# Performance work log

Measured on AMD Instinct MI355X. Metric: run time of the kernel, lower is better.

Reference implementation:

```python
import jax, jax.numpy as jnp
import numpy as np

NEG_SLOPE = 0.2

def _leaky(x):
    return jnp.where(x >= 0, x, NEG_SLOPE * x)

def _unigat(X, W, b, ae, av, pair_e, pair_v, num_v, num_e):
    # theta
    Xp = X @ W + b                                                    # [N, d]
    # v2e mean aggregation -> hyperedge features
    deg_e = jax.ops.segment_sum(jnp.ones(pair_e.shape, jnp.float32), pair_e, num_segments=num_e)
    Y = jax.ops.segment_sum(Xp[pair_v], pair_e, num_segments=num_e) / jnp.maximum(deg_e, 1.0)[:, None]  # [E, d]
    # GAT-style attention per incidence pair (edge term + node term), dropout=identity in eval
    s = _leaky((Y @ ae)[pair_e] + (Xp @ av)[pair_v])                  # [P]
    # segment softmax over edges incident to each node
    m = jax.ops.segment_max(s, pair_v, num_segments=num_v)
    ex = jnp.exp(s - m[pair_v])
    den = jax.ops.segment_sum(ex, pair_v, num_segments=num_v)
    alpha = ex / den[pair_v]                                          # [P]
    out = jax.ops.segment_sum(alpha[:, None] * Y[pair_e], pair_v, num_segments=num_v)  # [N, d]
    return jax.nn.elu(out)  # is_last=False everywhere -> ELU (use_bn=False)

def _multi_head(X, W, b, ae, av, pair_e, pair_v, num_v, num_e):
    # W:[H,din,d] b:[H,d] ae/av:[H,d]; concat heads on feature dim
    f = lambda Wh, bh, aeh, avh: _unigat(X, Wh, bh, aeh, avh, pair_e, pair_v, num_v, num_e)
    outs = jax.vmap(f)(W, b, ae, av)                                  # [H, N, d]
    return jnp.transpose(outs, (1, 0, 2)).reshape(X.shape[0], -1)     # [N, H*d]

def setup_inputs() -> dict:
    key = jax.random.key(0)
    ks = jax.random.split(key, 12)
    N, E, P = 100000, 20000, 1600000
    din, dh, H, C = 128, 64, 4, 40
    concat = 2
    inp = {
        "x0": jax.random.normal(ks[0], (N, din), jnp.float32),
        "x1": jax.random.normal(ks[1], (N, din), jnp.float32),
        "W1": jax.random.normal(ks[2], (H, din, dh), jnp.float32) * 0.05,
        "b1": jnp.zeros((H, dh), jnp.float32),
        "ae1": jax.random.normal(ks[3], (H, dh), jnp.float32) * 0.05,
        "av1": jax.random.normal(ks[4], (H, dh), jnp.float32) * 0.05,
        "W2": jax.random.normal(ks[5], (concat * dh * H, C), jnp.float32) * 0.05,
        "b2": jnp.zeros((C,), jnp.float32),
        "ae2": jax.random.normal(ks[6], (C,), jnp.float32) * 0.05,
        "av2": jax.random.normal(ks[7], (C,), jnp.float32) * 0.05,
        "pair_e": jax.random.randint(ks[8], (P,), 0, E, jnp.int32),
        "pair_v": jax.random.randint(ks[9], (P,), 0, N, jnp.int32),
        "num_v": N,
        "num_e": E,
    }
    return inp

def reference(x0, x1, W1, b1, ae1, av1, W2, b2, ae2, av2, pair_e, pair_v, num_v, num_e):
    # dropout layers are identity in eval mode
    h0 = _multi_head(x0, W1, b1, ae1, av1, pair_e, pair_v, num_v, num_e)
    h1 = _multi_head(x1, W1, b1, ae1, av1, pair_e, pair_v, num_v, num_e)
    h = jnp.concatenate([h0, h1], axis=-1)                            # [N, concat*H*dh]
    return _unigat(h, W2, b2, ae2, av2, pair_e, pair_v, num_v, num_e) # [N, C]
```

## Files before the change

### kernel.cpp

```cpp
#include <hip/hip_runtime.h>
#include <cstdint>
#include <cstddef>

static constexpr int DIN = 128;
static constexpr int DH = 64;
static constexpr int NH = 4;
static constexpr int DCAT = 512;
static constexpr int NC = 40;
static constexpr int E_CONST = 20000;
static constexpr int SH_V = 9, SUBD_V = 512;
static constexpr int SH_E = 7, SUBD_E = 128;
static constexpr int CHUNKA = 4096;

typedef unsigned short u16;
typedef __attribute__((ext_vector_type(4))) unsigned short u16x4;
typedef __attribute__((ext_vector_type(8))) unsigned short u16x8;
typedef __attribute__((ext_vector_type(8))) short bf16x8;
typedef __attribute__((ext_vector_type(4))) float f32x4;

static __device__ __forceinline__ float bf2f(u16 u) {
    union { unsigned int i; float f; } x;
    x.i = ((unsigned int)u) << 16;
    return x.f;
}
static __device__ __forceinline__ u16 f2bf(float f) {
    union { float f; unsigned int i; } x;
    x.f = f;
    unsigned int r = x.i + 0x7fffu + ((x.i >> 16) & 1u);
    return (u16)(r >> 16);
}


__global__ void k_hist2(const int* __restrict__ pv, const int* __restrict__ pe,
                        int* __restrict__ btot_v, int* __restrict__ btot_e, int P) {
    __shared__ int cv[256], ce[256];
    int tid = threadIdx.x;
    cv[tid] = 0; ce[tid] = 0;
    __syncthreads();
    int p0 = blockIdx.x * CHUNKA;
    #pragma unroll
    for (int j = 0; j < CHUNKA / 256; ++j) {
        int p = p0 + tid + j * 256;
        if (p < P) {
            atomicAdd(&cv[pv[p] >> SH_V], 1);
            atomicAdd(&ce[pe[p] >> SH_E], 1);
        }
    }
    __syncthreads();
    if (cv[tid]) atomicAdd(&btot_v[tid], cv[tid]);
    if (ce[tid]) atomicAdd(&btot_e[tid], ce[tid]);
}

__global__ void k_scan_small(int* __restrict__ a, int n) {
    __shared__ int wsum[16];
    __shared__ int carry_s;
    int tid = threadIdx.x;
    int lane = tid & 63;
    int w = tid >> 6;
    if (tid == 0) carry_s = 0;
    __syncthreads();
    for (int base = 0; base < n; base += 1024) {
        int i = base + tid;
        int v = (i < n) ? a[i] : 0;
        int x = v;
        #pragma unroll
        for (int off = 1; off < 64; off <<= 1) {
            int t = __shfl_up(x, off);
            if (lane >= off) x += t;
        }
        if (lane == 63) wsum[w] = x;
        __syncthreads();
        int woff = 0;
        for (int k = 0; k < w; ++k) woff += wsum[k];
        int carry = carry_s;
        if (i < n) a[i] = carry + woff + x - v;
        int tot = 0;
        for (int k = 0; k < 16; ++k) tot += wsum[k];
        __syncthreads();
        if (tid == 0) carry_s = carry + tot;
        __syncthreads();
    }
    if (tid == 0) a[n] = carry_s;
}

__global__ void k_scatter2way(const int* __restrict__ pv, const int* __restrict__ pe,
                              const int* __restrict__ bstart_v, const int* __restrict__ bstart_e,
                              int* __restrict__ cur_v, int* __restrict__ cur_e,
                              uint2* __restrict__ sorted_v, uint2* __restrict__ sorted_e, int P) {
    __shared__ int cv[256], ce[256], posv[256], pose[256];
    int tid = threadIdx.x;
    cv[tid] = 0; ce[tid] = 0;
    __syncthreads();
    int p0 = blockIdx.x * CHUNKA;
    int kv[CHUNKA / 256], ke[CHUNKA / 256];
    #pragma unroll
    for (int j = 0; j < CHUNKA / 256; ++j) {
        int p = p0 + tid + j * 256;
        if (p < P) {
            kv[j] = pv[p];
            ke[j] = pe[p];
            atomicAdd(&cv[kv[j] >> SH_V], 1);
            atomicAdd(&ce[ke[j] >> SH_E], 1);
        } else {
            kv[j] = -1;
            ke[j] = -1;
        }
    }
    __syncthreads();
    if (cv[tid]) posv[tid] = bstart_v[tid] + atomicAdd(&cur_v[tid], cv[tid]);
    if (ce[tid]) pose[tid] = bstart_e[tid] + atomicAdd(&cur_e[tid], ce[tid]);
    __syncthreads();
    #pragma unroll
    for (int j = 0; j < CHUNKA / 256; ++j) {
        if (kv[j] >= 0) {
            int iv = atomicAdd(&posv[kv[j] >> SH_V], 1);
            sorted_v[iv] = make_uint2((unsigned)kv[j], (unsigned)ke[j]);
            int ie = atomicAdd(&pose[ke[j] >> SH_E], 1);
            sorted_e[ie] = make_uint2((unsigned)ke[j], (unsigned)kv[j]);
        }
    }
}

template <int SUBD, int SH>
__global__ void k_build(const uint2* __restrict__ sorted, const int* __restrict__ bstart,
                        int* __restrict__ start_out, int* __restrict__ deg_out,
                        int* __restrict__ csr_out, int D) {
    __shared__ int deg[SUBD], pos[SUBD];
    int b = blockIdx.x;
    int tid = threadIdx.x;
    int base_key = b << SH;
    int s0 = bstart[b];
    int cnt = bstart[b + 1] - s0;
    for (int k = tid; k < SUBD; k += 256) deg[k] = 0;
    __syncthreads();
    for (int i = tid; i < cnt; i += 256)
        atomicAdd(&deg[(int)sorted[s0 + i].x - base_key], 1);
    __syncthreads();
    if (tid < 64) {
        int carry = 0;
        for (int base = 0; base < SUBD; base += 64) {
            int d = deg[base + tid];
            int x = d;
            #pragma unroll
            for (int off = 1; off < 64; off <<= 1) {
                int t = __shfl_up(x, off);
                if (tid >= off) x += t;
            }
            pos[base + tid] = carry + x - d;
            carry += __shfl(x, 63);
        }
    }
    __syncthreads();
    for (int k = tid; k < SUBD; k += 256) {
        int key = base_key + k;
        if (key < D) {
            start_out[key] = s0 + pos[k];
            deg_out[key] = deg[k];
        }
    }
    __syncthreads();
    for (int i = tid; i < cnt; i += 256) {
        uint2 pr = sorted[s0 + i];
        int loc = (int)pr.x - base_key;
        int idx = atomicAdd(&pos[loc], 1);
        csr_out[s0 + idx] = (int)pr.y;
    }
}


__global__ void k_wav(const float* __restrict__ W1, const float* __restrict__ b1,
                      const float* __restrict__ av1, float* __restrict__ wav,
                      float* __restrict__ bav) {
    int h = blockIdx.x;
    int k = threadIdx.x;
    float s = 0.f;
    for (int j = 0; j < DH; ++j) s += W1[(size_t)(h * DIN + k) * DH + j] * av1[h * DH + j];
    wav[h * DIN + k] = s;
    if (k == 0) {
        float t = 0.f;
        for (int j = 0; j < DH; ++j) t += b1[h * DH + j] * av1[h * DH + j];
        bav[h] = t;
    }
}

__global__ void k_build_wcatT(const float* __restrict__ W1, u16* __restrict__ WcatT) {
    int idx = blockIdx.x * 256 + threadIdx.x;
    if (idx >= 256 * DIN) return;
    int c = idx >> 7, k = idx & 127;
    int h = c >> 6, j = c & 63;
    WcatT[c * DIN + k] = f2bf(W1[((size_t)h * DIN + k) * DH + j]);
}

__global__ void k_build_w2T(const float* __restrict__ W2, u16* __restrict__ W2T) {
    int idx = blockIdx.x * 256 + threadIdx.x;
    if (idx >= 48 * DCAT) return;
    int c = idx >> 9, k = idx & 511;
    float v = (c < NC) ? W2[(size_t)k * NC + c] : 0.f;
    W2T[c * DCAT + k] = f2bf(v);
}

__global__ void k_conv(const float* __restrict__ X0, const float* __restrict__ X1,
                       const float* __restrict__ wav, const float* __restrict__ bav,
                       u16* __restrict__ Xbi, float* __restrict__ sv8, int N) {
    int wave = (blockIdx.x * blockDim.x + threadIdx.x) >> 6;
    int lane = threadIdx.x & 63;
    if (wave >= N) return;
    int xz = blockIdx.y;
    const float* X = xz ? X1 : X0;
    float2 a = *(const float2*)(X + (size_t)wave * DIN + lane * 2);
    unsigned int packed = (unsigned int)f2bf(a.x) | ((unsigned int)f2bf(a.y) << 16);
    *(unsigned int*)(Xbi + (size_t)wave * 256 + xz * 128 + lane * 2) = packed;
    float s[NH];
    #pragma unroll
    for (int h = 0; h < NH; ++h) {
        float2 wv = *(const float2*)(wav + h * DIN + lane * 2);
        float t = a.x * wv.x + a.y * wv.y;
        #pragma unroll
        for (int off = 32; off >= 1; off >>= 1) t += __shfl_xor(t, off);
        s[h] = t;
    }
    if (lane == 0) {
        #pragma unroll
        for (int h = 0; h < NH; ++h) sv8[(size_t)wave * 8 + h * 2 + xz] = s[h] + bav[h];
    }
}

__global__ void k_edge_mean1(const u16* __restrict__ Xbi, const int* __restrict__ start_e,
                             const int* __restrict__ deg_e, const int* __restrict__ csr_e_v,
                             u16* __restrict__ Xbar0, u16* __restrict__ Xbar1, int E) {
    int wave = (blockIdx.x * blockDim.x + threadIdx.x) >> 6;
    int lane = threadIdx.x & 63;
    if (wave >= E) return;
    int s = start_e[wave], t = s + deg_e[wave];
    int q = lane >> 4, c = lane & 15;
    float a0[8], a1[8];
    #pragma unroll
    for (int j = 0; j < 8; ++j) { a0[j] = 0.f; a1[j] = 0.f; }
    int i = s + q;
    u16x8 y0A = {0}, y1A = {0}, y0B = {0}, y1B = {0}, y0C = {0}, y1C = {0};
#define EM1_LOAD(Y0, Y1, IDX) { int v_ = csr_e_v[IDX]; \
        const u16* yp_ = Xbi + (size_t)v_ * 256 + c * 8; \
        Y0 = *(const u16x8*)yp_; Y1 = *(const u16x8*)(yp_ + 128); }
#define EM1_CONSUME(Y0, Y1) { \
        _Pragma("unroll") \
        for (int j = 0; j < 8; ++j) { a0[j] += bf2f(Y0[j]); a1[j] += bf2f(Y1[j]); } }
    if (i < t) EM1_LOAD(y0A, y1A, i);
    if (i + 4 < t) EM1_LOAD(y0B, y1B, i + 4);
    if (i + 8 < t) EM1_LOAD(y0C, y1C, i + 8);
    for (; i + 8 < t; i += 12) {
        EM1_CONSUME(y0A, y1A);
        if (i + 12 < t) EM1_LOAD(y0A, y1A, i + 12);
        EM1_CONSUME(y0B, y1B);
        if (i + 16 < t) EM1_LOAD(y0B, y1B, i + 16);
        EM1_CONSUME(y0C, y1C);
        if (i + 20 < t) EM1_LOAD(y0C, y1C, i + 20);
    }
    if (i < t) EM1_CONSUME(y0A, y1A);
    if (i + 4 < t) EM1_CONSUME(y0B, y1B);
#undef EM1_LOAD
#undef EM1_CONSUME
    #pragma unroll
    for (int j = 0; j < 8; ++j) {
        a0[j] += __shfl_xor(a0[j], 16);
        a0[j] += __shfl_xor(a0[j], 32);
        a1[j] += __shfl_xor(a1[j], 16);
        a1[j] += __shfl_xor(a1[j], 32);
    }
    int deg = t - s;
    float inv = 1.f / (float)(deg > 1 ? deg : 1);
    if (q == 0) {
        u16x8 r0, r1;
        #pragma unroll
        for (int j = 0; j < 8; ++j) { r0[j] = f2bf(a0[j] * inv); r1[j] = f2bf(a1[j] * inv); }
        *(u16x8*)(Xbar0 + (size_t)wave * DIN + c * 8) = r0;
        *(u16x8*)(Xbar1 + (size_t)wave * DIN + c * 8) = r1;
    }
}

template <int KDIM, int NTILES, int DOTMODE>
__global__ __launch_bounds__(256) void k_gemm_mfma(const u16* __restrict__ A0,
                                                   const u16* __restrict__ A1, int M,
                                                   const u16* __restrict__ Bt,
                                                   const float* __restrict__ bias,
                                                   u16* __restrict__ out0, u16* __restrict__ out1,
                                                   int ldo, int ncols,
                                                   const float* __restrict__ dvec,
                                                   float* __restrict__ dout) {
    constexpr int LDB = KDIM + 8;
    __shared__ u16 Bs[NTILES * 16 * LDB];
    const u16* A = blockIdx.z ? A1 : A0;
    u16* out = blockIdx.z ? out1 : out0;
    int tid = threadIdx.x;
    int colbase = blockIdx.y * NTILES * 16;
    const u16* Btblk = Bt + (size_t)colbase * KDIM;
    for (int idx = tid * 4; idx < NTILES * 16 * KDIM; idx += 256 * 4) {
        int c = idx / KDIM, k = idx % KDIM;
        *(u16x4*)&Bs[c * LDB + k] = *(const u16x4*)(Btblk + c * KDIM + k);
    }
    __syncthreads();
    int w = tid >> 6, lane = tid & 63;
    int r0 = blockIdx.x * 64 + w * 16;
    int arow = r0 + (lane & 15);
    bool avalid = arow < M;
    const u16* ap = A + (size_t)arow * KDIM + (lane >> 4) * 8;
    f32x4 acc[NTILES];
    #pragma unroll
    for (int nt = 0; nt < NTILES; ++nt) acc[nt] = (f32x4){0.f, 0.f, 0.f, 0.f};
    #pragma unroll
    for (int k0 = 0; k0 < KDIM; k0 += 32) {
        bf16x8 a = (bf16x8)(short)0;
        if (avalid) a = *(const bf16x8*)(ap + k0);
        #pragma unroll
        for (int nt = 0; nt < NTILES; ++nt) {
            bf16x8 b = *(const bf16x8*)&Bs[(nt * 16 + (lane & 15)) * LDB + k0 + (lane >> 4) * 8];
            acc[nt] = __builtin_amdgcn_mfma_f32_16x16x32_bf16(a, b, acc[nt], 0, 0, 0);
        }
    }
    #pragma unroll
    for (int j = 0; j < 4; ++j) {
        int row = r0 + (lane >> 4) * 4 + j;
        float pA = 0.f, pB = 0.f;
        #pragma unroll
        for (int nt = 0; nt < NTILES; ++nt) {
            int col = colbase + nt * 16 + (lane & 15);
            bool cok = col < ncols;
            float val = cok ? acc[nt][j] + bias[col] : 0.f;
            if (DOTMODE == 1) {
                float dv = dvec[col];
                if (nt < NTILES / 2) pA += val * dv; else pB += val * dv;
            } else if (DOTMODE == 2) {
                pA += cok ? val * dvec[col] : 0.f;
            }
            if (row < M && cok) out[(size_t)row * ldo + col] = f2bf(val);
        }
        if (DOTMODE) {
            pA += __shfl_xor(pA, 1);
            pA += __shfl_xor(pA, 2);
            pA += __shfl_xor(pA, 4);
            pA += __shfl_xor(pA, 8);
            if (DOTMODE == 1) {
                pB += __shfl_xor(pB, 1);
                pB += __shfl_xor(pB, 2);
                pB += __shfl_xor(pB, 4);
                pB += __shfl_xor(pB, 8);
            }
            if ((lane & 15) == 0 && row < M) {
                if (DOTMODE == 1) {
                    int hbase = blockIdx.y * 2;
                    int z = blockIdx.z;
                    dout[(size_t)row * 8 + hbase * 2 + z] = pA;
                    dout[(size_t)row * 8 + (hbase + 1) * 2 + z] = pB;
                } else {
                    dout[row] = pA;
                }
            }
        }
    }
}

__global__ void k_node_pass1(const u16* __restrict__ Ycat, const float* __restrict__ se8,
                             const float* __restrict__ sv8, const int* __restrict__ start_v,
                             const int* __restrict__ deg_v, const int* __restrict__ csr_v_e,
                             u16* __restrict__ hbuf, int N) {
    int wave = (blockIdx.x * blockDim.x + threadIdx.x) >> 6;
    int lane = threadIdx.x & 63;
    if (wave >= N) return;
    int p0 = start_v[wave], p1 = p0 + deg_v[wave];
    int g = lane >> 5;
    int c = lane & 31;
    int h = c >> 3;
    u16* orow = hbuf + (size_t)wave * DCAT + c * 8;
    if (p1 == p0) {
        if (g == 0) {
            u16x8 z8 = {0, 0, 0, 0, 0, 0, 0, 0};
            *(u16x8*)orow = z8;
            *(u16x8*)(orow + 256) = z8;
        }
        return;
    }
    float sv0 = sv8[(size_t)wave * 8 + h * 2];
    float sv1 = sv8[(size_t)wave * 8 + h * 2 + 1];
    float den0 = 0.f, den1 = 0.f;
    float a0[8], a1[8];
    #pragma unroll
    for (int j = 0; j < 8; ++j) { a0[j] = 0.f; a1[j] = 0.f; }
    for (int i = p0 + g; i < p1; i += 2) {
        int e = csr_v_e[i];
        float2 s2 = *(const float2*)(se8 + e * 8 + h * 2);
        float x0 = s2.x + sv0;
        float x1 = s2.y + sv1;
        x0 = fmaxf(x0, 0.2f * x0);
        x1 = fmaxf(x1, 0.2f * x1);
        float e0 = __expf(x0);
        float e1 = __expf(x1);
        den0 += e0;
        den1 += e1;
        const u16* yp = Ycat + (size_t)e * 512 + c * 8;
        u16x8 q0 = *(const u16x8*)yp;
        u16x8 q1 = *(const u16x8*)(yp + 256);
        #pragma unroll
        for (int j = 0; j < 8; ++j) { a0[j] += e0 * bf2f(q0[j]); a1[j] += e1 * bf2f(q1[j]); }
    }
    den0 += __shfl_xor(den0, 32);
    den1 += __shfl_xor(den1, 32);
    #pragma unroll
    for (int j = 0; j < 8; ++j) {
        a0[j] += __shfl_xor(a0[j], 32);
        a1[j] += __shfl_xor(a1[j], 32);
    }
    float i0 = 1.f / den0, i1 = 1.f / den1;
    u16x8 r0, r1;
    #pragma unroll
    for (int j = 0; j < 8; ++j) {
        float o0 = a0[j] * i0;
        float o1 = a1[j] * i1;
        o0 = o0 > 0.f ? o0 : __expf(o0) - 1.f;
        o1 = o1 > 0.f ? o1 : __expf(o1) - 1.f;
        r0[j] = f2bf(o0);
        r1[j] = f2bf(o1);
    }
    if (g == 0) {
        *(u16x8*)orow = r0;
        *(u16x8*)(orow + 256) = r1;
    }
}


__global__ void k_edge_mean2(const u16* __restrict__ Xp2b, const int* __restrict__ start_e,
                             const int* __restrict__ deg_ea, const int* __restrict__ csr_e_v,
                             u16* __restrict__ Y2b, const float* __restrict__ ae2,
                             float* __restrict__ se2, int E) {
    int wave = (blockIdx.x * blockDim.x + threadIdx.x) >> 6;
    int lane = threadIdx.x & 63;
    if (wave >= E) return;
    int s = start_e[wave], t = s + deg_ea[wave];
    int g = lane >> 4, c = lane & 15;
    bool act = c < 10;
    float acc[4];
    #pragma unroll
    for (int j = 0; j < 4; ++j) acc[j] = 0.f;
    for (int i = s + g; i < t; i += 4) {
        int v = csr_e_v[i];
        if (act) {
            u16x4 y = *(const u16x4*)(Xp2b + (size_t)v * NC + c * 4);
            acc[0] += bf2f(y.x);
            acc[1] += bf2f(y.y);
            acc[2] += bf2f(y.z);
            acc[3] += bf2f(y.w);
        }
    }
    #pragma unroll
    for (int j = 0; j < 4; ++j) {
        acc[j] += __shfl_xor(acc[j], 16);
        acc[j] += __shfl_xor(acc[j], 32);
    }
    int deg = t - s;
    float inv = 1.f / (float)(deg > 1 ? deg : 1);
    float p = 0.f;
    if (act) {
        float4 ae = *(const float4*)(ae2 + c * 4);
        float y0 = acc[0] * inv, y1 = acc[1] * inv, y2 = acc[2] * inv, y3 = acc[3] * inv;
        p = y0 * ae.x + y1 * ae.y + y2 * ae.z + y3 * ae.w;
        if (g == 0) {
            u16x4 r = {f2bf(y0), f2bf(y1), f2bf(y2), f2bf(y3)};
            *(u16x4*)(Y2b + (size_t)wave * NC + c * 4) = r;
        }
    }
    #pragma unroll
    for (int off = 8; off >= 1; off >>= 1) p += __shfl_xor(p, off);
    if (lane == 0) se2[wave] = p;
}

__global__ void k_node_pass2(const u16* __restrict__ Y2b, const float* __restrict__ se2,
                             const float* __restrict__ sv2, const int* __restrict__ start_v,
                             const int* __restrict__ deg_va, const int* __restrict__ csr_v_e,
                             float* __restrict__ out, int N) {
    int wave = (blockIdx.x * blockDim.x + threadIdx.x) >> 6;
    int lane = threadIdx.x & 63;
    if (wave >= N) return;
    int s = start_v[wave], t = s + deg_va[wave];
    int g = lane >> 4, c = lane & 15;
    bool act = c < 10;
    float* orow = out + (size_t)wave * NC;
    if (t == s) {
        if (g == 0 && act) *(float4*)(orow + c * 4) = make_float4(0.f, 0.f, 0.f, 0.f);
        return;
    }
    float svv = sv2[wave];
    float den = 0.f;
    float acc[4];
    #pragma unroll
    for (int j = 0; j < 4; ++j) acc[j] = 0.f;
    for (int i = s + g; i < t; i += 4) {
        int e = csr_v_e[i];
        float x = se2[e] + svv;
        x = fmaxf(x, 0.2f * x);
        float ex = __expf(x);
        den += ex;
        if (act) {
            u16x4 y = *(const u16x4*)(Y2b + (size_t)e * NC + c * 4);
            acc[0] += ex * bf2f(y.x);
            acc[1] += ex * bf2f(y.y);
            acc[2] += ex * bf2f(y.z);
            acc[3] += ex * bf2f(y.w);
        }
    }
    den += __shfl_xor(den, 16);
    den += __shfl_xor(den, 32);
    #pragma unroll
    for (int j = 0; j < 4; ++j) {
        acc[j] += __shfl_xor(acc[j], 16);
        acc[j] += __shfl_xor(acc[j], 32);
    }
    if (g == 0 && act) {
        float inv = 1.f / den;
        float4 o;
        float* op = &o.x;
        #pragma unroll
        for (int j = 0; j < 4; ++j) {
            float v = acc[j] * inv;
            op[j] = v > 0.f ? v : __expf(v) - 1.f;
        }
        *(float4*)(orow + c * 4) = o;
    }
}

extern "C" void kernel_launch(void* const* d_in, const int* in_sizes, int n_in,
                              void* d_out, int out_size, void* d_ws, size_t ws_size,
                              hipStream_t stream) {
    const float* x0 = (const float*)d_in[0];
    const float* x1 = (const float*)d_in[1];
    const float* W1 = (const float*)d_in[2];
    const float* b1 = (const float*)d_in[3];
    const float* ae1 = (const float*)d_in[4];
    const float* av1 = (const float*)d_in[5];
    const float* W2 = (const float*)d_in[6];
    const float* b2 = (const float*)d_in[7];
    const float* ae2 = (const float*)d_in[8];
    const float* av2 = (const float*)d_in[9];
    const int* pe = (const int*)d_in[10];
    const int* pv = (const int*)d_in[11];

    const int N = in_sizes[0] / DIN;
    const int P = in_sizes[10];
    const int E = E_CONST;
    const int NBKT_V = (N + SUBD_V - 1) / SUBD_V;
    const int NBKT_E = (E + SUBD_E - 1) / SUBD_E;

    char* base = (char*)d_ws;
    auto alloc = [&](size_t bytes) -> void* {
        void* p = (void*)base;
        base += (bytes + 255) & ~(size_t)255;
        return p;
    };
    u16* Xbi = (u16*)alloc((size_t)N * 256 * 2);
    u16* hbuf = (u16*)alloc((size_t)N * DCAT * 2);
    u16* Xbar0 = (u16*)alloc((size_t)E * DIN * 2);
    u16* Xbar1 = (u16*)alloc((size_t)E * DIN * 2);
    u16* Ycat = (u16*)alloc((size_t)E * 512 * 2);
    u16* Xp2b = (u16*)alloc((size_t)N * NC * 2);
    u16* Y2b = (u16*)alloc((size_t)E * NC * 2);
    float* se8 = (float*)alloc((size_t)E * 8 * 4);
    float* se2 = (float*)alloc((size_t)E * 4);
    float* sv8 = (float*)alloc((size_t)N * 8 * 4);
    float* sv2 = (float*)alloc((size_t)N * 4);
    float* wav = (float*)alloc((size_t)NH * DIN * 4);
    float* bav = (float*)alloc((size_t)NH * 4);
    u16* WcatT = (u16*)alloc((size_t)256 * DIN * 2);
    u16* W2T = (u16*)alloc((size_t)48 * DCAT * 2);
    uint2* sorted_v = (uint2*)alloc((size_t)P * 8);
    uint2* sorted_e = (uint2*)alloc((size_t)P * 8);
    int* start_v = (int*)alloc((size_t)N * 4);
    int* deg_v = (int*)alloc((size_t)N * 4);
    int* start_e = (int*)alloc((size_t)E * 4);
    int* deg_e = (int*)alloc((size_t)E * 4);
    int* csr_v_e = (int*)alloc((size_t)P * 4);
    int* csr_e_v = (int*)alloc((size_t)P * 4);
    char* zstart = base;
    int* bstart_v = (int*)alloc((size_t)(NBKT_V + 1) * 4);
    int* bstart_e = (int*)alloc((size_t)(NBKT_E + 1) * 4);
    int* cur_v = (int*)alloc((size_t)256 * 4);
    int* cur_e = (int*)alloc((size_t)256 * 4);
    size_t zbytes = (size_t)(base - zstart);

    if ((size_t)(base - (char*)d_ws) > ws_size) return;

    hipMemsetAsync(zstart, 0, zbytes, stream);

    dim3 b256(256);
    int nA = (P + CHUNKA - 1) / CHUNKA;
    k_hist2<<<nA, b256, 0, stream>>>(pv, pe, bstart_v, bstart_e, P);
    k_scan_small<<<1, 1024, 0, stream>>>(bstart_v, NBKT_V);
    k_scan_small<<<1, 1024, 0, stream>>>(bstart_e, NBKT_E);
    k_scatter2way<<<nA, b256, 0, stream>>>(pv, pe, bstart_v, bstart_e, cur_v, cur_e,
                                           sorted_v, sorted_e, P);
    k_build<SUBD_V, SH_V><<<NBKT_V, b256, 0, stream>>>(sorted_v, bstart_v, start_v, deg_v,
                                                       csr_v_e, N);
    k_build<SUBD_E, SH_E><<<NBKT_E, b256, 0, stream>>>(sorted_e, bstart_e, start_e, deg_e,
                                                       csr_e_v, E);

    k_wav<<<NH, DIN, 0, stream>>>(W1, b1, av1, wav, bav);
    k_build_wcatT<<<(256 * DIN + 255) / 256, b256, 0, stream>>>(W1, WcatT);
    k_build_w2T<<<(48 * DCAT + 255) / 256, b256, 0, stream>>>(W2, W2T);

    int gN4 = (N + 3) / 4;
    int gE4 = (E + 3) / 4;
    dim3 gconv(gN4, 2);
    k_conv<<<gconv, b256, 0, stream>>>(x0, x1, wav, bav, Xbi, sv8, N);

    k_edge_mean1<<<gE4, b256, 0, stream>>>(Xbi, start_e, deg_e, csr_e_v, Xbar0, Xbar1, E);
    dim3 g1((E + 63) / 64, 2, 2);
    k_gemm_mfma<DIN, 8, 1><<<g1, b256, 0, stream>>>(Xbar0, Xbar1, E, WcatT, b1,
                                                    Ycat, Ycat + 256, 512, 256, ae1, se8);
    k_node_pass1<<<gN4, b256, 0, stream>>>(Ycat, se8, sv8, start_v, deg_v, csr_v_e, hbuf, N);

    dim3 g2((N + 63) / 64, 1, 1);
    k_gemm_mfma<DCAT, 3, 2><<<g2, b256, 0, stream>>>(hbuf, hbuf, N, W2T, b2, Xp2b, Xp2b,
                                                     NC, NC, av2, sv2);
    k_edge_mean2<<<gE4, b256, 0, stream>>>(Xp2b, start_e, deg_e, csr_e_v, Y2b, ae2, se2, E);
    k_node_pass2<<<gN4, b256, 0, stream>>>(Y2b, se2, sv2, start_v, deg_v, csr_v_e,
                                           (float*)d_out, N);
}
```

Baseline: 675.4 us.

## Sub-bucket CSR build by secondary key to order neighbor lists

```diff
diff --git a/kernel.cpp b/kernel.cpp
--- a/kernel.cpp
+++ b/kernel.cpp
@@ -10,6 +10,10 @@
 static constexpr int E_CONST = 20000;
 static constexpr int SH_V = 9, SUBD_V = 512;
 static constexpr int SH_E = 7, SUBD_E = 128;
+static constexpr int ECH = 11, NSUB_E = 10;
+static constexpr int VCH = 12, NSUB_V = 25;
+static constexpr int NKV = 196 * NSUB_E;
+static constexpr int NKE = 157 * NSUB_V;
 static constexpr int CHUNKA = 4096;
 
 typedef unsigned short u16;
@@ -29,26 +33,32 @@
     unsigned int r = x.i + 0x7fffu + ((x.i >> 16) & 1u);
     return (u16)(r >> 16);
 }
+static __device__ __forceinline__ int keyV(int v, int e) { return (v >> SH_V) * NSUB_E + (e >> ECH); }
+static __device__ __forceinline__ int keyE(int e, int v) { return (e >> SH_E) * NSUB_V + (v >> VCH); }
 
 
 __global__ void k_hist2(const int* __restrict__ pv, const int* __restrict__ pe,
                         int* __restrict__ btot_v, int* __restrict__ btot_e, int P) {
-    __shared__ int cv[256], ce[256];
+    __shared__ int cv[NKV], ce[NKE];
     int tid = threadIdx.x;
-    cv[tid] = 0; ce[tid] = 0;
+    for (int k = tid; k < NKV; k += 256) cv[k] = 0;
+    for (int k = tid; k < NKE; k += 256) ce[k] = 0;
     __syncthreads();
     int p0 = blockIdx.x * CHUNKA;
     #pragma unroll
     for (int j = 0; j < CHUNKA / 256; ++j) {
         int p = p0 + tid + j * 256;
         if (p < P) {
-            atomicAdd(&cv[pv[p] >> SH_V], 1);
-            atomicAdd(&ce[pe[p] >> SH_E], 1);
-        }
-    }
-    __syncthreads();
-    if (cv[tid]) atomicAdd(&btot_v[tid], cv[tid]);
-    if (ce[tid]) atomicAdd(&btot_e[tid], ce[tid]);
+            int v = pv[p], e = pe[p];
+            atomicAdd(&cv[keyV(v, e)], 1);
+            atomicAdd(&ce[keyE(e, v)], 1);
+        }
+    }
+    __syncthreads();
+    for (int k = tid; k < NKV; k += 256)
+        if (cv[k]) atomicAdd(&btot_v[k], cv[k]);
+    for (int k = tid; k < NKE; k += 256)
+        if (ce[k]) atomicAdd(&btot_e[k], ce[k]);
 }
 
 __global__ void k_scan_small(int* __restrict__ a, int n) {
@@ -87,9 +97,10 @@
                               const int* __restrict__ bstart_v, const int* __restrict__ bstart_e,
                               int* __restrict__ cur_v, int* __restrict__ cur_e,
                               uint2* __restrict__ sorted_v, uint2* __restrict__ sorted_e, int P) {
-    __shared__ int cv[256], ce[256], posv[256], pose[256];
+    __shared__ int cv[NKV], posv[NKV], ce[NKE], pose[NKE];
     int tid = threadIdx.x;
-    cv[tid] = 0; ce[tid] = 0;
+    for (int k = tid; k < NKV; k += 256) cv[k] = 0;
+    for (int k = tid; k < NKE; k += 256) ce[k] = 0;
     __syncthreads();
     int p0 = blockIdx.x * CHUNKA;
     int kv[CHUNKA / 256], ke[CHUNKA / 256];
@@ -99,29 +110,31 @@
         if (p < P) {
             kv[j] = pv[p];
             ke[j] = pe[p];
-            atomicAdd(&cv[kv[j] >> SH_V], 1);
-            atomicAdd(&ce[ke[j] >> SH_E], 1);
+            atomicAdd(&cv[keyV(kv[j], ke[j])], 1);
+            atomicAdd(&ce[keyE(ke[j], kv[j])], 1);
         } else {
             kv[j] = -1;
             ke[j] = -1;
         }
     }
     __syncthreads();
-    if (cv[tid]) posv[tid] = bstart_v[tid] + atomicAdd(&cur_v[tid], cv[tid]);
-    if (ce[tid]) pose[tid] = bstart_e[tid] + atomicAdd(&cur_e[tid], ce[tid]);
+    for (int k = tid; k < NKV; k += 256)
+        if (cv[k]) posv[k] = bstart_v[k] + atomicAdd(&cur_v[k], cv[k]);
+    for (int k = tid; k < NKE; k += 256)
+        if (ce[k]) pose[k] = bstart_e[k] + atomicAdd(&cur_e[k], ce[k]);
     __syncthreads();
     #pragma unroll
     for (int j = 0; j < CHUNKA / 256; ++j) {
         if (kv[j] >= 0) {
-            int iv = atomicAdd(&posv[kv[j] >> SH_V], 1);
+            int iv = atomicAdd(&posv[keyV(kv[j], ke[j])], 1);
             sorted_v[iv] = make_uint2((unsigned)kv[j], (unsigned)ke[j]);
-            int ie = atomicAdd(&pose[ke[j] >> SH_E], 1);
+            int ie = atomicAdd(&pose[keyE(ke[j], kv[j])], 1);
             sorted_e[ie] = make_uint2((unsigned)ke[j], (unsigned)kv[j]);
         }
     }
 }
 
-template <int SUBD, int SH>
+template <int SUBD, int SH, int NSUB>
 __global__ void k_build(const uint2* __restrict__ sorted, const int* __restrict__ bstart,
                         int* __restrict__ start_out, int* __restrict__ deg_out,
                         int* __restrict__ csr_out, int D) {
@@ -129,11 +142,14 @@
     int b = blockIdx.x;
     int tid = threadIdx.x;
     int base_key = b << SH;
-    int s0 = bstart[b];
-    int cnt = bstart[b + 1] - s0;
+    int s0 = bstart[b * NSUB];
+    int cnt = bstart[(b + 1) * NSUB] - s0;
     for (int k = tid; k < SUBD; k += 256) deg[k] = 0;
     __syncthreads();
-    for (int i = tid; i < cnt; i += 256)
+    int span = (cnt + 255) / 256;
+    int i0 = tid * span;
+    int i1 = i0 + span < cnt ? i0 + span : cnt;
+    for (int i = i0; i < i1; ++i)
         atomicAdd(&deg[(int)sorted[s0 + i].x - base_key], 1);
     __syncthreads();
     if (tid < 64) {
@@ -159,7 +175,7 @@
         }
     }
     __syncthreads();
-    for (int i = tid; i < cnt; i += 256) {
+    for (int i = i0; i < i1; ++i) {
         uint2 pr = sorted[s0 + i];
         int loc = (int)pr.x - base_key;
         int idx = atomicAdd(&pos[loc], 1);
@@ -577,10 +593,10 @@
     int* csr_v_e = (int*)alloc((size_t)P * 4);
     int* csr_e_v = (int*)alloc((size_t)P * 4);
     char* zstart = base;
-    int* bstart_v = (int*)alloc((size_t)(NBKT_V + 1) * 4);
-    int* bstart_e = (int*)alloc((size_t)(NBKT_E + 1) * 4);
-    int* cur_v = (int*)alloc((size_t)256 * 4);
-    int* cur_e = (int*)alloc((size_t)256 * 4);
+    int* bstart_v = (int*)alloc((size_t)(NKV + 1) * 4);
+    int* bstart_e = (int*)alloc((size_t)(NKE + 1) * 4);
+    int* cur_v = (int*)alloc((size_t)NKV * 4);
+    int* cur_e = (int*)alloc((size_t)NKE * 4);
     size_t zbytes = (size_t)(base - zstart);
 
     if ((size_t)(base - (char*)d_ws) > ws_size) return;
@@ -590,14 +606,14 @@
     dim3 b256(256);
     int nA = (P + CHUNKA - 1) / CHUNKA;
     k_hist2<<<nA, b256, 0, stream>>>(pv, pe, bstart_v, bstart_e, P);
-    k_scan_small<<<1, 1024, 0, stream>>>(bstart_v, NBKT_V);
-    k_scan_small<<<1, 1024, 0, stream>>>(bstart_e, NBKT_E);
+    k_scan_small<<<1, 1024, 0, stream>>>(bstart_v, NKV);
+    k_scan_small<<<1, 1024, 0, stream>>>(bstart_e, NKE);
     k_scatter2way<<<nA, b256, 0, stream>>>(pv, pe, bstart_v, bstart_e, cur_v, cur_e,
                                            sorted_v, sorted_e, P);
-    k_build<SUBD_V, SH_V><<<NBKT_V, b256, 0, stream>>>(sorted_v, bstart_v, start_v, deg_v,
-                                                       csr_v_e, N);
-    k_build<SUBD_E, SH_E><<<NBKT_E, b256, 0, stream>>>(sorted_e, bstart_e, start_e, deg_e,
-                                                       csr_e_v, E);
+    k_build<SUBD_V, SH_V, NSUB_E><<<NBKT_V, b256, 0, stream>>>(sorted_v, bstart_v, start_v,
+                                                               deg_v, csr_v_e, N);
+    k_build<SUBD_E, SH_E, NSUB_V><<<NBKT_E, b256, 0, stream>>>(sorted_e, bstart_e, start_e,
+                                                               deg_e, csr_e_v, E);
 
     k_wav<<<NH, DIN, 0, stream>>>(W1, b1, av1, wav, bav);
     k_build_wcatT<<<(256 * DIN + 255) / 256, b256, 0, stream>>>(W1, WcatT);
```

New measurement: 722.2 us. 6.9% more time.

## Order CSR neighbor lists by coarse neighbor-index bucket for gather locality

Applied to the files above, without the earlier changes.

```diff
diff --git a/kernel.cpp b/kernel.cpp
--- a/kernel.cpp
+++ b/kernel.cpp
@@ -10,6 +10,8 @@
 static constexpr int E_CONST = 20000;
 static constexpr int SH_V = 9, SUBD_V = 512;
 static constexpr int SH_E = 7, SUBD_E = 128;
+static constexpr int ECH = 11, NSUB_E = 10;
+static constexpr int VCH = 12, NSUB_V = 25;
 static constexpr int CHUNKA = 4096;
 
 typedef unsigned short u16;
@@ -121,48 +123,75 @@
     }
 }
 
-template <int SUBD, int SH>
-__global__ void k_build(const uint2* __restrict__ sorted, const int* __restrict__ bstart,
-                        int* __restrict__ start_out, int* __restrict__ deg_out,
-                        int* __restrict__ csr_out, int D) {
-    __shared__ int deg[SUBD], pos[SUBD];
+template <int SUBD, int SH, int NSUB, int CSH>
+__global__ __launch_bounds__(256) void k_build_ord(const uint2* __restrict__ sorted,
+                                                   const int* __restrict__ bstart,
+                                                   int* __restrict__ start_out,
+                                                   int* __restrict__ deg_out,
+                                                   int* __restrict__ csr_out, int D) {
+    constexpr int NK2 = SUBD * NSUB;
+    constexpr int STRIP = (NK2 + 255) / 256;
+    __shared__ int cnt[NK2];
+    __shared__ int wsum[4];
     int b = blockIdx.x;
     int tid = threadIdx.x;
     int base_key = b << SH;
     int s0 = bstart[b];
-    int cnt = bstart[b + 1] - s0;
-    for (int k = tid; k < SUBD; k += 256) deg[k] = 0;
-    __syncthreads();
-    for (int i = tid; i < cnt; i += 256)
-        atomicAdd(&deg[(int)sorted[s0 + i].x - base_key], 1);
-    __syncthreads();
-    if (tid < 64) {
-        int carry = 0;
-        for (int base = 0; base < SUBD; base += 64) {
-            int d = deg[base + tid];
-            int x = d;
-            #pragma unroll
-            for (int off = 1; off < 64; off <<= 1) {
-                int t = __shfl_up(x, off);
-                if (tid >= off) x += t;
-            }
-            pos[base + tid] = carry + x - d;
-            carry += __shfl(x, 63);
-        }
-    }
-    __syncthreads();
-    for (int k = tid; k < SUBD; k += 256) {
-        int key = base_key + k;
+    int cntN = bstart[b + 1] - s0;
+    for (int k = tid; k < NK2; k += 256) cnt[k] = 0;
+    __syncthreads();
+    for (int i = tid; i < cntN; i += 256) {
+        uint2 pr = sorted[s0 + i];
+        int k2 = ((int)pr.x - base_key) * NSUB + ((int)pr.y >> CSH);
+        atomicAdd(&cnt[k2], 1);
+    }
+    __syncthreads();
+    int local[STRIP];
+    int sum = 0;
+    int t0 = tid * STRIP;
+    #pragma unroll
+    for (int j = 0; j < STRIP; ++j) {
+        int idx = t0 + j;
+        local[j] = (idx < NK2) ? cnt[idx] : 0;
+        sum += local[j];
+    }
+    int lane = tid & 63, w = tid >> 6;
+    int x = sum;
+    #pragma unroll
+    for (int off = 1; off < 64; off <<= 1) {
+        int t = __shfl_up(x, off);
+        if (lane >= off) x += t;
+    }
+    if (lane == 63) wsum[w] = x;
+    __syncthreads();
+    int woff = 0;
+    for (int k = 0; k < w; ++k) woff += wsum[k];
+    int run = woff + x - sum;
+    __syncthreads();
+    #pragma unroll
+    for (int j = 0; j < STRIP; ++j) {
+        int idx = t0 + j;
+        if (idx < NK2) {
+            int tmp = local[j];
+            cnt[idx] = run;
+            run += tmp;
+        }
+    }
+    __syncthreads();
+    for (int loc = tid; loc < SUBD; loc += 256) {
+        int key = base_key + loc;
         if (key < D) {
-            start_out[key] = s0 + pos[k];
-            deg_out[key] = deg[k];
-        }
-    }
-    __syncthreads();
-    for (int i = tid; i < cnt; i += 256) {
+            int st = cnt[loc * NSUB];
+            int en = (loc == SUBD - 1) ? cntN : cnt[(loc + 1) * NSUB];
+            start_out[key] = s0 + st;
+            deg_out[key] = en - st;
+        }
+    }
+    __syncthreads();
+    for (int i = tid; i < cntN; i += 256) {
         uint2 pr = sorted[s0 + i];
-        int loc = (int)pr.x - base_key;
-        int idx = atomicAdd(&pos[loc], 1);
+        int k2 = ((int)pr.x - base_key) * NSUB + ((int)pr.y >> CSH);
+        int idx = atomicAdd(&cnt[k2], 1);
         csr_out[s0 + idx] = (int)pr.y;
     }
 }
@@ -594,10 +623,12 @@
     k_scan_small<<<1, 1024, 0, stream>>>(bstart_e, NBKT_E);
     k_scatter2way<<<nA, b256, 0, stream>>>(pv, pe, bstart_v, bstart_e, cur_v, cur_e,
                                            sorted_v, sorted_e, P);
-    k_build<SUBD_V, SH_V><<<NBKT_V, b256, 0, stream>>>(sorted_v, bstart_v, start_v, deg_v,
-                                                       csr_v_e, N);
-    k_build<SUBD_E, SH_E><<<NBKT_E, b256, 0, stream>>>(sorted_e, bstart_e, start_e, deg_e,
-                                                       csr_e_v, E);
+    k_build_ord<SUBD_V, SH_V, NSUB_E, ECH><<<NBKT_V, b256, 0, stream>>>(sorted_v, bstart_v,
+                                                                        start_v, deg_v,
+                                                                        csr_v_e, N);
+    k_build_ord<SUBD_E, SH_E, NSUB_V, VCH><<<NBKT_E, b256, 0, stream>>>(sorted_e, bstart_e,
+                                                                        start_e, deg_e,
+                                                                        csr_e_v, E);
 
     k_wav<<<NH, DIN, 0, stream>>>(W1, b1, av1, wav, bav);
     k_build_wcatT<<<(256 * DIN + 255) / 256, b256, 0, stream>>>(W1, WcatT);
```

Result: no change. 666.3 us (-1.3%).
